# Kernel tuning notes

Measured on AMD Instinct MI355X. Metric: run time of the kernel, lower is better.

## Reference

```python
import jax, jax.numpy as jnp
import numpy as np

IN_F = 1024
OUT_F = 1024
R = 16
NUM_USERS = 10000
NUM_ITEMS = 10000
BATCH = 4096
SCALING = 32.0 / 16.0  # lora_alpha / r


def setup_inputs() -> dict:
    key = jax.random.key(0)
    ks = jax.random.split(key, 9)
    return {
        "x": jax.random.normal(ks[0], (BATCH, IN_F), dtype=jnp.float32),
        "user_indices": jax.random.randint(ks[1], (BATCH,), 0, NUM_USERS, dtype=jnp.int32),
        "item_indices": jax.random.randint(ks[2], (BATCH,), 0, NUM_ITEMS, dtype=jnp.int32),
        "W_base": jax.random.normal(ks[3], (OUT_F, IN_F), dtype=jnp.float32) * 0.02,
        "b_base": jax.random.normal(ks[4], (OUT_F,), dtype=jnp.float32) * 0.02,
        "A": jax.random.normal(ks[5], (R, IN_F), dtype=jnp.float32) * 0.02,
        "B_user": jax.random.normal(ks[6], (NUM_USERS, OUT_F, R), dtype=jnp.float32) * 0.02,
        "B_item": jax.random.normal(ks[7], (NUM_ITEMS, OUT_F, R), dtype=jnp.float32) * 0.02,
        "W_common": jax.random.normal(ks[8], (OUT_F, R), dtype=jnp.float32) * 0.02,
    }


def reference(x, user_indices, item_indices, W_base, b_base, A, B_user, B_item, W_common):
    # base linear: [B, out]
    base = x @ W_base.T + b_base
    # lora_A (dropout p=0 -> identity): [B, r]
    a = x @ A.T
    # gather per-row LoRA-B matrices: [B, out, r]
    Bu = B_user[user_indices]
    Bi = B_item[item_indices]
    # batched low-rank matmuls + shared common projection
    user_part = jnp.einsum("bor,br->bo", Bu, a)
    item_part = jnp.einsum("bor,br->bo", Bi, a)
    common_part = a @ W_common.T
    return base + SCALING * (user_part + item_part + common_part)
```

## Files before the change

kernel.cpp:

```cpp
#include <hip/hip_runtime.h>
#include <hip/hip_bf16.h>
#include <cstdint>
#include <cstddef>

typedef __attribute__((ext_vector_type(8))) __bf16 bf16x8;
typedef __attribute__((ext_vector_type(4))) __bf16 bf16x4;
typedef __attribute__((ext_vector_type(4))) float f32x4;

#define BATCH 4096
#define IN_FEAT 1024
#define OUT_FEAT 1024
#define RNK 16
#define SCALE 2.0f

__global__ __launch_bounds__(256) void prep_kernel(
    const float* __restrict__ x, const float* __restrict__ A,
    const float* __restrict__ W, const float* __restrict__ Wc,
    float* __restrict__ a_out, __bf16* __restrict__ x_bf,
    __bf16* __restrict__ w_bf)
{
    __shared__ float xs[IN_FEAT];
    const int b = blockIdx.x;
    const int t = threadIdx.x;
    const int k0 = t * 4;

    if (b < OUT_FEAT) {
        float4 wv = *reinterpret_cast<const float4*>(&W[(size_t)b * IN_FEAT + k0]);
        float cx = 0.f, cy = 0.f, cz = 0.f, cw = 0.f;
        #pragma unroll
        for (int r = 0; r < RNK; ++r) {
            const float wcr = Wc[b * RNK + r];
            const float4 av = *reinterpret_cast<const float4*>(&A[r * IN_FEAT + k0]);
            cx += wcr * av.x; cy += wcr * av.y; cz += wcr * av.z; cw += wcr * av.w;
        }
        bf16x4 hw;
        hw[0] = (__bf16)(wv.x + SCALE * cx);
        hw[1] = (__bf16)(wv.y + SCALE * cy);
        hw[2] = (__bf16)(wv.z + SCALE * cz);
        hw[3] = (__bf16)(wv.w + SCALE * cw);
        *reinterpret_cast<bf16x4*>(&w_bf[(size_t)b * IN_FEAT + k0]) = hw;
    }

    const float4 v = *reinterpret_cast<const float4*>(&x[(size_t)b * IN_FEAT + k0]);
    xs[k0 + 0] = v.x; xs[k0 + 1] = v.y; xs[k0 + 2] = v.z; xs[k0 + 3] = v.w;
    bf16x4 h;
    h[0] = (__bf16)v.x; h[1] = (__bf16)v.y; h[2] = (__bf16)v.z; h[3] = (__bf16)v.w;
    *reinterpret_cast<bf16x4*>(&x_bf[(size_t)b * IN_FEAT + k0]) = h;
    __syncthreads();

    const int r = t >> 4;
    const int l16 = t & 15;
    const float* __restrict__ Ar = &A[r * IN_FEAT];
    float s = 0.f;
    #pragma unroll 8
    for (int j = 0; j < IN_FEAT / 16; ++j) {
        const int k = l16 + 16 * j;
        s += xs[k] * Ar[k];
    }
    s += __shfl_xor(s, 8);
    s += __shfl_xor(s, 4);
    s += __shfl_xor(s, 2);
    s += __shfl_xor(s, 1);
    if (l16 == 0) a_out[b * RNK + r] = s;
}

#define BM 64
#define BN 64
#define BK 64
#define LDK 72

__global__ __launch_bounds__(256) void fused_kernel(
    const __bf16* __restrict__ x_bf, const __bf16* __restrict__ w_bf,
    const float* __restrict__ a_buf,
    const int* __restrict__ uidx, const int* __restrict__ iidx,
    const float* __restrict__ b_base,
    const float* __restrict__ B_user, const float* __restrict__ B_item,
    float* __restrict__ out)
{
    __shared__ __align__(16) __bf16 xs[BM * LDK];
    __shared__ __align__(16) __bf16 wsh[BN * LDK];
    __shared__ __align__(16) float a_s[BM * RNK];
    __shared__ int u_s[BM];
    __shared__ int i_s[BM];

    const int t = threadIdx.x;

    const int bid = blockIdx.y * gridDim.x + blockIdx.x;
    const int nid = (bid & 7) * 128 + (bid >> 3);
    const int o0 = (nid & 15) * BN;
    const int b0 = (nid >> 4) * BM;

    if (t < BM) {
        u_s[t] = uidx[b0 + t];
        i_s[t] = iidx[b0 + t];
    }
    *reinterpret_cast<float4*>(&a_s[t * 4]) =
        *reinterpret_cast<const float4*>(&a_buf[(size_t)b0 * RNK + t * 4]);

    const int w  = t >> 6;
    const int wr = w >> 1;
    const int wc = w & 1;
    const int l  = t & 63;
    const int lr = l & 15;
    const int lg = l >> 4;

    const int srow  = t >> 2;
    const int skoff = (t & 3) * 16;

    f32x4 acc[2][2] = {};

    #pragma unroll
    for (int kt = 0; kt < IN_FEAT / BK; ++kt) {
        __syncthreads();
        {
            const uint4* g = reinterpret_cast<const uint4*>(
                &x_bf[(size_t)(b0 + srow) * IN_FEAT + kt * BK + skoff]);
            uint4 v0 = g[0], v1 = g[1];
            *reinterpret_cast<uint4*>(&xs[srow * LDK + skoff]) = v0;
            *reinterpret_cast<uint4*>(&xs[srow * LDK + skoff + 8]) = v1;
            const uint4* gw = reinterpret_cast<const uint4*>(
                &w_bf[(size_t)(o0 + srow) * IN_FEAT + kt * BK + skoff]);
            uint4 w0 = gw[0], w1 = gw[1];
            *reinterpret_cast<uint4*>(&wsh[srow * LDK + skoff]) = w0;
            *reinterpret_cast<uint4*>(&wsh[srow * LDK + skoff + 8]) = w1;
        }
        __syncthreads();

        const int nn = kt >> 3;
        const int mm = (kt >> 2) & 1;
        const int ii = kt & 3;
        const int ol = wc * 32 + nn * 16 + lr;
        const int bl = wr * 32 + mm * 16 + lg * 4 + ii;
        const size_t u  = (size_t)u_s[bl];
        const size_t iv = (size_t)i_s[bl];
        const f32x4* bu = reinterpret_cast<const f32x4*>(
            &B_user[(u * OUT_FEAT + (size_t)(o0 + ol)) * RNK]);
        const f32x4* bi = reinterpret_cast<const f32x4*>(
            &B_item[(iv * OUT_FEAT + (size_t)(o0 + ol)) * RNK]);
        f32x4 gu0 = bu[0], gu1 = bu[1], gu2 = bu[2], gu3 = bu[3];
        f32x4 gi0 = bi[0], gi1 = bi[1], gi2 = bi[2], gi3 = bi[3];

        #pragma unroll
        for (int kk = 0; kk < BK; kk += 32) {
            bf16x8 af0 = *reinterpret_cast<const bf16x8*>(&xs[(wr * 32 + 0 + lr) * LDK + kk + lg * 8]);
            bf16x8 af1 = *reinterpret_cast<const bf16x8*>(&xs[(wr * 32 + 16 + lr) * LDK + kk + lg * 8]);
            bf16x8 bf0 = *reinterpret_cast<const bf16x8*>(&wsh[(wc * 32 + 0 + lr) * LDK + kk + lg * 8]);
            bf16x8 bf1 = *reinterpret_cast<const bf16x8*>(&wsh[(wc * 32 + 16 + lr) * LDK + kk + lg * 8]);
            acc[0][0] = __builtin_amdgcn_mfma_f32_16x16x32_bf16(af0, bf0, acc[0][0], 0, 0, 0);
            acc[0][1] = __builtin_amdgcn_mfma_f32_16x16x32_bf16(af0, bf1, acc[0][1], 0, 0, 0);
            acc[1][0] = __builtin_amdgcn_mfma_f32_16x16x32_bf16(af1, bf0, acc[1][0], 0, 0, 0);
            acc[1][1] = __builtin_amdgcn_mfma_f32_16x16x32_bf16(af1, bf1, acc[1][1], 0, 0, 0);
        }

        {
            const f32x4* av4 = reinterpret_cast<const f32x4*>(&a_s[bl * RNK]);
            float lora = 0.f;
            {
                const f32x4 s0 = gu0 + gi0, a0 = av4[0];
                lora += s0[0]*a0[0] + s0[1]*a0[1] + s0[2]*a0[2] + s0[3]*a0[3];
                const f32x4 s1 = gu1 + gi1, a1 = av4[1];
                lora += s1[0]*a1[0] + s1[1]*a1[1] + s1[2]*a1[2] + s1[3]*a1[3];
                const f32x4 s2 = gu2 + gi2, a2 = av4[2];
                lora += s2[0]*a2[0] + s2[1]*a2[1] + s2[2]*a2[2] + s2[3]*a2[3];
                const f32x4 s3 = gu3 + gi3, a3 = av4[3];
                lora += s3[0]*a3[0] + s3[1]*a3[1] + s3[2]*a3[2] + s3[3]*a3[3];
            }
            acc[mm][nn][ii] += SCALE * lora;
        }
    }

    #pragma unroll
    for (int n = 0; n < 2; ++n) {
        const int o = o0 + wc * 32 + n * 16 + lr;
        const float bb = b_base[o];
        #pragma unroll
        for (int m = 0; m < 2; ++m) {
            #pragma unroll
            for (int i = 0; i < 4; ++i) {
                const int bl2 = wr * 32 + m * 16 + lg * 4 + i;
                out[(size_t)(b0 + bl2) * OUT_FEAT + o] = acc[m][n][i] + bb;
            }
        }
    }
}

extern "C" void kernel_launch(void* const* d_in, const int* in_sizes, int n_in,
                              void* d_out, int out_size, void* d_ws, size_t ws_size,
                              hipStream_t stream) {
    const float* x        = (const float*)d_in[0];
    const int*   uidx     = (const int*)d_in[1];
    const int*   iidx     = (const int*)d_in[2];
    const float* W_base   = (const float*)d_in[3];
    const float* b_base   = (const float*)d_in[4];
    const float* A        = (const float*)d_in[5];
    const float* B_user   = (const float*)d_in[6];
    const float* B_item   = (const float*)d_in[7];
    const float* W_common = (const float*)d_in[8];
    float* out = (float*)d_out;

    float*  a_buf = (float*)d_ws;
    __bf16* x_bf  = (__bf16*)((char*)d_ws + (256 << 10));
    __bf16* w_bf  = (__bf16*)((char*)d_ws + (256 << 10) + (8 << 20));

    prep_kernel<<<BATCH, 256, 0, stream>>>(x, A, W_base, W_common, a_buf, x_bf, w_bf);

    dim3 grid(OUT_FEAT / BN, BATCH / BM);
    fused_kernel<<<grid, 256, 0, stream>>>(x_bf, w_bf, a_buf, uidx, iidx,
                                           b_base, B_user, B_item, out);
}
```

Before: 132.5 us.

## Double-buffer LDS tiles with register prefetch and read LoRA-A values from global

Converts the GEMM main loop to a double-buffered LDS scheme. The next k-tile is loaded from global into registers before the MFMAs and written into the alternate buffer afterward, which removes one barrier per iteration and overlaps global latency with compute. It also drops the shared a_s staging and reads the per-row rank vector directly from global alongside the B gathers. The cost is doubled LDS footprint and higher register pressure from the prefetch registers.

```diff
diff --git a/kernel.cpp b/kernel.cpp
--- a/kernel.cpp
+++ b/kernel.cpp
@@ -77,9 +77,8 @@
     const float* __restrict__ B_user, const float* __restrict__ B_item,
     float* __restrict__ out)
 {
-    __shared__ __align__(16) __bf16 xs[BM * LDK];
-    __shared__ __align__(16) __bf16 wsh[BN * LDK];
-    __shared__ __align__(16) float a_s[BM * RNK];
+    __shared__ __align__(16) __bf16 xs[2][BM * LDK];
+    __shared__ __align__(16) __bf16 wsh[2][BM * LDK];
     __shared__ int u_s[BM];
     __shared__ int i_s[BM];
 
@@ -94,8 +93,6 @@
         u_s[t] = uidx[b0 + t];
         i_s[t] = iidx[b0 + t];
     }
-    *reinterpret_cast<float4*>(&a_s[t * 4]) =
-        *reinterpret_cast<const float4*>(&a_buf[(size_t)b0 * RNK + t * 4]);
 
     const int w  = t >> 6;
     const int wr = w >> 1;
@@ -108,23 +105,33 @@
     const int skoff = (t & 3) * 16;
 
     f32x4 acc[2][2] = {};
+    uint4 sx0, sx1, sw0, sw1;
+
+    #define STAGE_LOAD(kt) do {                                                      \
+        const __bf16* px_ = &x_bf[(size_t)(b0 + srow) * IN_FEAT + (kt) * BK + skoff];\
+        sx0 = *reinterpret_cast<const uint4*>(px_);                                  \
+        sx1 = *reinterpret_cast<const uint4*>(px_ + 8);                              \
+        const __bf16* pw_ = &w_bf[(size_t)(o0 + srow) * IN_FEAT + (kt) * BK + skoff];\
+        sw0 = *reinterpret_cast<const uint4*>(pw_);                                  \
+        sw1 = *reinterpret_cast<const uint4*>(pw_ + 8);                              \
+    } while (0)
+
+    #define STAGE_WRITE(buf) do {                                                   \
+        *reinterpret_cast<uint4*>(&xs[(buf)][srow * LDK + skoff])      = sx0;        \
+        *reinterpret_cast<uint4*>(&xs[(buf)][srow * LDK + skoff + 8])  = sx1;        \
+        *reinterpret_cast<uint4*>(&wsh[(buf)][srow * LDK + skoff])     = sw0;        \
+        *reinterpret_cast<uint4*>(&wsh[(buf)][srow * LDK + skoff + 8]) = sw1;        \
+    } while (0)
+
+    STAGE_LOAD(0);
+    STAGE_WRITE(0);
+    __syncthreads();
 
     #pragma unroll
     for (int kt = 0; kt < IN_FEAT / BK; ++kt) {
-        __syncthreads();
-        {
-            const uint4* g = reinterpret_cast<const uint4*>(
-                &x_bf[(size_t)(b0 + srow) * IN_FEAT + kt * BK + skoff]);
-            uint4 v0 = g[0], v1 = g[1];
-            *reinterpret_cast<uint4*>(&xs[srow * LDK + skoff]) = v0;
-            *reinterpret_cast<uint4*>(&xs[srow * LDK + skoff + 8]) = v1;
-            const uint4* gw = reinterpret_cast<const uint4*>(
-                &w_bf[(size_t)(o0 + srow) * IN_FEAT + kt * BK + skoff]);
-            uint4 w0 = gw[0], w1 = gw[1];
-            *reinterpret_cast<uint4*>(&wsh[srow * LDK + skoff]) = w0;
-            *reinterpret_cast<uint4*>(&wsh[srow * LDK + skoff + 8]) = w1;
-        }
-        __syncthreads();
+        const int cur = kt & 1;
+
+        if (kt < IN_FEAT / BK - 1) STAGE_LOAD(kt + 1);
 
         const int nn = kt >> 3;
         const int mm = (kt >> 2) & 1;
@@ -137,36 +144,40 @@
             &B_user[(u * OUT_FEAT + (size_t)(o0 + ol)) * RNK]);
         const f32x4* bi = reinterpret_cast<const f32x4*>(
             &B_item[(iv * OUT_FEAT + (size_t)(o0 + ol)) * RNK]);
+        const f32x4* pa = reinterpret_cast<const f32x4*>(
+            &a_buf[(size_t)(b0 + bl) * RNK]);
         f32x4 gu0 = bu[0], gu1 = bu[1], gu2 = bu[2], gu3 = bu[3];
         f32x4 gi0 = bi[0], gi1 = bi[1], gi2 = bi[2], gi3 = bi[3];
+        f32x4 ga0 = pa[0], ga1 = pa[1], ga2 = pa[2], ga3 = pa[3];
 
         #pragma unroll
         for (int kk = 0; kk < BK; kk += 32) {
-            bf16x8 af0 = *reinterpret_cast<const bf16x8*>(&xs[(wr * 32 + 0 + lr) * LDK + kk + lg * 8]);
-            bf16x8 af1 = *reinterpret_cast<const bf16x8*>(&xs[(wr * 32 + 16 + lr) * LDK + kk + lg * 8]);
-            bf16x8 bf0 = *reinterpret_cast<const bf16x8*>(&wsh[(wc * 32 + 0 + lr) * LDK + kk + lg * 8]);
-            bf16x8 bf1 = *reinterpret_cast<const bf16x8*>(&wsh[(wc * 32 + 16 + lr) * LDK + kk + lg * 8]);
+            bf16x8 af0 = *reinterpret_cast<const bf16x8*>(&xs[cur][(wr * 32 + 0 + lr) * LDK + kk + lg * 8]);
+            bf16x8 af1 = *reinterpret_cast<const bf16x8*>(&xs[cur][(wr * 32 + 16 + lr) * LDK + kk + lg * 8]);
+            bf16x8 bf0 = *reinterpret_cast<const bf16x8*>(&wsh[cur][(wc * 32 + 0 + lr) * LDK + kk + lg * 8]);
+            bf16x8 bf1 = *reinterpret_cast<const bf16x8*>(&wsh[cur][(wc * 32 + 16 + lr) * LDK + kk + lg * 8]);
             acc[0][0] = __builtin_amdgcn_mfma_f32_16x16x32_bf16(af0, bf0, acc[0][0], 0, 0, 0);
             acc[0][1] = __builtin_amdgcn_mfma_f32_16x16x32_bf16(af0, bf1, acc[0][1], 0, 0, 0);
             acc[1][0] = __builtin_amdgcn_mfma_f32_16x16x32_bf16(af1, bf0, acc[1][0], 0, 0, 0);
             acc[1][1] = __builtin_amdgcn_mfma_f32_16x16x32_bf16(af1, bf1, acc[1][1], 0, 0, 0);
         }
 
+        if (kt < IN_FEAT / BK - 1) STAGE_WRITE(cur ^ 1);
+
         {
-            const f32x4* av4 = reinterpret_cast<const f32x4*>(&a_s[bl * RNK]);
             float lora = 0.f;
-            {
-                const f32x4 s0 = gu0 + gi0, a0 = av4[0];
-                lora += s0[0]*a0[0] + s0[1]*a0[1] + s0[2]*a0[2] + s0[3]*a0[3];
-                const f32x4 s1 = gu1 + gi1, a1 = av4[1];
-                lora += s1[0]*a1[0] + s1[1]*a1[1] + s1[2]*a1[2] + s1[3]*a1[3];
-                const f32x4 s2 = gu2 + gi2, a2 = av4[2];
-                lora += s2[0]*a2[0] + s2[1]*a2[1] + s2[2]*a2[2] + s2[3]*a2[3];
-                const f32x4 s3 = gu3 + gi3, a3 = av4[3];
-                lora += s3[0]*a3[0] + s3[1]*a3[1] + s3[2]*a3[2] + s3[3]*a3[3];
-            }
+            const f32x4 s0 = gu0 + gi0;
+            lora += s0[0]*ga0[0] + s0[1]*ga0[1] + s0[2]*ga0[2] + s0[3]*ga0[3];
+            const f32x4 s1 = gu1 + gi1;
+            lora += s1[0]*ga1[0] + s1[1]*ga1[1] + s1[2]*ga1[2] + s1[3]*ga1[3];
+            const f32x4 s2 = gu2 + gi2;
+            lora += s2[0]*ga2[0] + s2[1]*ga2[1] + s2[2]*ga2[2] + s2[3]*ga2[3];
+            const f32x4 s3 = gu3 + gi3;
+            lora += s3[0]*ga3[0] + s3[1]*ga3[1] + s3[2]*ga3[2] + s3[3]*ga3[3];
             acc[mm][nn][ii] += SCALE * lora;
         }
+
+        __syncthreads();
     }
 
     #pragma unroll
@@ -182,6 +193,9 @@
             }
         }
     }
+
+    #undef STAGE_LOAD
+    #undef STAGE_WRITE
 }
 
 extern "C" void kernel_launch(void* const* d_in, const int* in_sizes, int n_in,
```

Result: no change. 135.1 us (+2.0%).
